# Kernel tuning notes

Hardware: AMD Instinct MI355X
Metric: run time of the kernel (lower is better)

The kernel has to match this reference:

```python
import jax, jax.numpy as jnp
import numpy as np

NDIR = 6      # build_tree.num_directions()
IDIM = 256
ODIM = 512
B, L, NCH = 8, 4096, 8192


def setup_inputs() -> dict:
    key = jax.random.key(0)
    ks = jax.random.split(key, 9)
    last = jax.random.normal(ks[0], (B, NCH, IDIM), dtype=jnp.float32)
    child_l = jax.random.randint(ks[1], (L,), 0, NCH, dtype=jnp.int32)
    child_r = jax.random.randint(ks[2], (L,), 0, NCH, dtype=jnp.int32)
    vec = jax.random.randint(ks[3], (B, L), 0, NCH, dtype=jnp.int32)
    drev = jax.random.randint(ks[4], (NCH,), 0, 2, dtype=jnp.int32)
    dmap = jax.random.randint(ks[5], (NCH,), 0, NDIR, dtype=jnp.int32)
    # merge FC params: ndir independent Linear(2*idim -> odim) + PReLU(init=relu_weight)
    scale = 1.0 / np.sqrt(2 * IDIM)
    W_merge = jax.random.uniform(ks[6], (NDIR, ODIM, 2 * IDIM), jnp.float32, -scale, scale)
    b_merge = jax.random.uniform(ks[7], (NDIR, ODIM), jnp.float32, -scale, scale)
    alpha_merge = jnp.full((NDIR,), 0.005, dtype=jnp.float32)  # PReLU weight (relu_weight)
    return {"last": last, "W_merge": W_merge, "b_merge": b_merge,
            "alpha_merge": alpha_merge, "child_l": child_l, "child_r": child_r,
            "vec": vec, "drev": drev, "dmap": dmap}


def reference(last, W_merge, b_merge, alpha_merge, child_l, child_r, vec, drev, dmap):
    # child gathers: [B, L, idim]
    lch = last[:, child_l]
    rch = last[:, child_r]
    # per-element direction-reverse blending
    d = drev[vec][:, :, None].astype(last.dtype)          # [B, L, 1]
    a = lch * (1.0 - d) + rch * d
    b = rch * (1.0 - d) + lch * d
    ans = jnp.concatenate([a, b], axis=-1)                # [B, L, 2*idim]
    # routed merge: compute all ndir linears, then select per element (ndir is small)
    y_all = jnp.einsum('bli,doi->bldo', ans, W_merge) + b_merge   # [B, L, ndir, odim]
    dir_idx = dmap[vec]                                   # [B, L] in [0, ndir)
    y = jnp.take_along_axis(y_all, dir_idx[:, :, None, None], axis=2)[:, :, 0]  # [B, L, odim]
    alpha = alpha_merge[dir_idx][:, :, None]              # per-element PReLU slope
    return jnp.where(y > 0, y, alpha * y)
```

## Files before the change

### kernel.cpp

```cpp
#include <hip/hip_runtime.h>
#include <hip/hip_bf16.h>

#define BB 8
#define LL 4096
#define NCH 8192
#define IDIM 256
#define KDIM 512
#define ODIM 512
#define NDIR 6
#define TOT (BB * LL)

typedef short short8 __attribute__((ext_vector_type(8)));
typedef float floatx4 __attribute__((ext_vector_type(4)));

#define WS_LAST_OFF (64 + 2 * TOT)
#define LAST_ELEMS (BB * NCH * IDIM)
#define W_ELEMS (NDIR * ODIM * KDIM)
#define N_LAST8 (LAST_ELEMS / 8)
#define N_W8 (W_ELEMS / 8)

__device__ inline void async_copy16(const void* g, void* l) {
  __builtin_amdgcn_global_load_lds(
      (const __attribute__((address_space(1))) void*)g,
      (__attribute__((address_space(3))) void*)l, 16, 0, 0);
}

__device__ inline void cvt8(const float* __restrict__ src,
                            __hip_bfloat16* __restrict__ dst, int i) {
  const floatx4* s = (const floatx4*)src;
  floatx4 a = s[2 * i];
  floatx4 b = s[2 * i + 1];
  union { short8 v; __hip_bfloat16 h[8]; } u;
  u.h[0] = __float2bfloat16(a[0]); u.h[1] = __float2bfloat16(a[1]);
  u.h[2] = __float2bfloat16(a[2]); u.h[3] = __float2bfloat16(a[3]);
  u.h[4] = __float2bfloat16(b[0]); u.h[5] = __float2bfloat16(b[1]);
  u.h[6] = __float2bfloat16(b[2]); u.h[7] = __float2bfloat16(b[3]);
  ((short8*)dst)[i] = u.v;
}

__global__ __launch_bounds__(256) void prep_kernel(
    const float* __restrict__ last, const float* __restrict__ W,
    const int* __restrict__ vec, const int* __restrict__ dmap,
    int* __restrict__ ws) {
  __hip_bfloat16* last_bf = (__hip_bfloat16*)(ws + WS_LAST_OFF);
  __hip_bfloat16* W_bf = last_bf + LAST_ELEMS;
  int gid = blockIdx.x * 256 + threadIdx.x;
  if (gid < N_LAST8) {
    cvt8(last, last_bf, gid);
  } else if (gid < N_LAST8 + N_W8) {
    cvt8(W, W_bf, gid - N_LAST8);
  } else {
    __shared__ int lcnt[8];
    int tid = threadIdx.x;
    if (tid < 8) lcnt[tid] = 0;
    __syncthreads();
    int lin = gid - (N_LAST8 + N_W8);
    int dir = dmap[vec[lin]] & 7;
    atomicAdd(&lcnt[dir], 1);
    __syncthreads();
    if (tid < 8 && lcnt[tid]) atomicAdd(&ws[tid], lcnt[tid]);
  }
}

__global__ void scan_kernel(int* __restrict__ ws) {
  if (threadIdx.x == 0) {
    int s = 0;
    for (int d = 0; d < 8; ++d) { ws[16 + d] = s; s += ws[d]; }
  }
}

__global__ __launch_bounds__(256) void scatter_kernel(
    const int* __restrict__ vec, const int* __restrict__ child_l,
    const int* __restrict__ child_r, const int* __restrict__ drev,
    const int* __restrict__ dmap, int* __restrict__ ws) {
  __shared__ int lcnt[8];
  __shared__ int gbase[8];
  int* fill = ws + 8;
  const int* base = ws + 16;
  int* idx = ws + 64;
  int* rows = ws + 64 + TOT;

  int tid = threadIdx.x;
  if (tid < 8) lcnt[tid] = 0;
  __syncthreads();

  int lin = blockIdx.x * 256 + tid;
  int l = lin & (LL - 1);
  int v = vec[lin];
  int dir = dmap[v] & 7;
  int sw = drev[v];
  int cl = child_l[l];
  int cr = child_r[l];
  int r0 = sw ? cr : cl;
  int r1 = sw ? cl : cr;
  int pos = atomicAdd(&lcnt[dir], 1);
  __syncthreads();
  if (tid < 8) gbase[tid] = lcnt[tid] ? atomicAdd(&fill[tid], lcnt[tid]) : 0;
  __syncthreads();
  int slot = base[dir] + gbase[dir] + pos;
  idx[slot] = lin;
  rows[slot] = r0 | (r1 << 16);
}

__global__ __launch_bounds__(256) void gemm_kernel(
    const float* __restrict__ bias, const float* __restrict__ alpha_m,
    const int* __restrict__ ws, float* __restrict__ out) {
  __shared__ __hip_bfloat16 Als[128 * 64];
  __shared__ __hip_bfloat16 Bls[128 * 64];

  const int mt = blockIdx.y;
  const int nt = blockIdx.x;
  int d = -1, count = 0, off = 0, m_base = 0;
  {
    int tb = 0;
    for (int dd = 0; dd < NDIR; ++dd) {
      int c = ws[dd];
      int ntile = (c + 127) >> 7;
      if (mt < tb + ntile) { d = dd; count = c; off = ws[16 + dd]; m_base = (mt - tb) * 128; break; }
      tb += ntile;
    }
  }
  if (d < 0) return;

  const int* idx = ws + 64;
  const int* rows = ws + 64 + TOT;
  const __hip_bfloat16* last_bf = (const __hip_bfloat16*)(ws + WS_LAST_OFF);
  const __hip_bfloat16* W_bf = last_bf + LAST_ELEMS;

  const int tid = threadIdx.x;
  const int wave = __builtin_amdgcn_readfirstlane(tid >> 6);
  const int lane = tid & 63;
  const int lane15 = lane & 15;
  const int quad = lane >> 4;
  const int wm = wave >> 1;
  const int wn = wave & 1;
  const int n_blk = nt * 128;

  const __hip_bfloat16* ap0[4];
  const __hip_bfloat16* ap1[4];
  const __hip_bfloat16* bp[4];
  int ldsrow[4];
#pragma unroll
  for (int i = 0; i < 4; ++i) {
    int sr = wave * 32 + i * 8 + (lane >> 3);
    ldsrow[i] = (wave * 32 + i * 8) * 64;
    int lr = m_base + sr;
    if (lr >= count) lr = count - 1;
    int lin = idx[off + lr] & (TOT - 1);
    int rr = rows[off + lr];
    int b = lin >> 12;
    int r0 = rr & (NCH - 1);
    int r1 = (rr >> 16) & (NCH - 1);
    int xu = ((lane & 7) ^ (sr & 7)) * 8;
    ap0[i] = last_bf + (long long)(b * NCH + r0) * IDIM + xu;
    ap1[i] = last_bf + (long long)(b * NCH + r1) * IDIM + xu;
    int xuB = xu;
    bp[i] = W_bf + (long long)(d * ODIM + n_blk + sr) * KDIM + xuB;
  }

  floatx4 acc[4][4] = {};
  const int lx = lane15 & 7;

#pragma unroll
  for (int kt = 0; kt < 8; ++kt) {
    __syncthreads();
    const int ko = (kt & 3) * 64;
#pragma unroll
    for (int i = 0; i < 4; ++i) {
      const __hip_bfloat16* ga = (kt < 4 ? ap0[i] : ap1[i]) + ko;
      async_copy16(ga, &Als[ldsrow[i]]);
    }
#pragma unroll
    for (int i = 0; i < 4; ++i) {
      async_copy16(bp[i] + kt * 64, &Bls[ldsrow[i]]);
    }
    __syncthreads();

#pragma unroll
    for (int s = 0; s < 2; ++s) {
      const int xcol = ((quad + 4 * s) ^ lx) * 8;
      short8 a[4], b[4];
#pragma unroll
      for (int i = 0; i < 4; ++i)
        a[i] = *(const short8*)&Als[(wm * 64 + i * 16 + lane15) * 64 + xcol];
#pragma unroll
      for (int j = 0; j < 4; ++j)
        b[j] = *(const short8*)&Bls[(wn * 64 + j * 16 + lane15) * 64 + xcol];
#pragma unroll
      for (int i = 0; i < 4; ++i)
#pragma unroll
        for (int j = 0; j < 4; ++j)
          acc[i][j] = __builtin_amdgcn_mfma_f32_16x16x32_bf16(a[i], b[j], acc[i][j], 0, 0, 0);
    }
  }

  const float alpha = alpha_m[d];
  float bj[4];
#pragma unroll
  for (int j = 0; j < 4; ++j)
    bj[j] = bias[d * ODIM + n_blk + wn * 64 + j * 16 + lane15];

#pragma unroll
  for (int i = 0; i < 4; ++i) {
#pragma unroll
    for (int reg = 0; reg < 4; ++reg) {
      int row_id = m_base + wm * 64 + i * 16 + quad * 4 + reg;
      if (row_id >= count) continue;
      int lin = idx[off + row_id] & (TOT - 1);
      float* orow = out + (long long)lin * ODIM + n_blk + wn * 64;
#pragma unroll
      for (int j = 0; j < 4; ++j) {
        float y = acc[i][j][reg] + bj[j];
        y = y > 0.f ? y : alpha * y;
        orow[j * 16 + lane15] = y;
      }
    }
  }
}

extern "C" void kernel_launch(void* const* d_in, const int* in_sizes, int n_in,
                              void* d_out, int out_size, void* d_ws, size_t ws_size,
                              hipStream_t stream) {
  const float* last = (const float*)d_in[0];
  const float* W = (const float*)d_in[1];
  const float* bias = (const float*)d_in[2];
  const float* alpha = (const float*)d_in[3];
  const int* child_l = (const int*)d_in[4];
  const int* child_r = (const int*)d_in[5];
  const int* vec = (const int*)d_in[6];
  const int* drev = (const int*)d_in[7];
  const int* dmap = (const int*)d_in[8];

  int* ws = (int*)d_ws;

  hipMemsetAsync(ws, 0, 64 * sizeof(int), stream);
  int prep_blocks = (N_LAST8 + N_W8 + TOT) / 256;
  prep_kernel<<<prep_blocks, 256, 0, stream>>>(last, W, vec, dmap, ws);
  scan_kernel<<<1, 64, 0, stream>>>(ws);
  scatter_kernel<<<TOT / 256, 256, 0, stream>>>(vec, child_l, child_r, drev, dmap, ws);
  dim3 grid(ODIM / 128, TOT / 128 + NDIR, 1);
  gemm_kernel<<<grid, 256, 0, stream>>>(bias, alpha, ws, (float*)d_out);
}
```

Baseline: 169.3 us.

## Pack gathered child rows into per-direction bf16 buffer and double-buffer GEMM K loop

Replaces full conversion of the input tensor to bf16 with a pack kernel that gathers only the needed left/right child rows, converts them, and writes them contiguously per direction slot. The scan and prep launches are removed, with slot positions computed directly in the scatter kernel using per-direction regions of size TOT. The GEMM now streams contiguous packed A rows with a two-stage LDS double buffer over 32-wide K tiles. This trades a large sparse workspace and an extra write of the gathered activations for simpler, coalesced GEMM loads and overlap of loads with MFMA work.

Measured after the change: 176.6 us. 1.04x slower.

```diff
diff --git a/kernel.cpp b/kernel.cpp
--- a/kernel.cpp
+++ b/kernel.cpp
@@ -13,60 +13,16 @@
 typedef short short8 __attribute__((ext_vector_type(8)));
 typedef float floatx4 __attribute__((ext_vector_type(4)));
 
-#define WS_LAST_OFF (64 + 2 * TOT)
-#define LAST_ELEMS (BB * NCH * IDIM)
+#define IDX_OFF (64 + 2 * TOT)
+#define PACKA_OFF_INTS (64 + (2 + NDIR) * TOT)
+#define PACKA_ELEMS ((long long)NDIR * TOT * KDIM)
 #define W_ELEMS (NDIR * ODIM * KDIM)
-#define N_LAST8 (LAST_ELEMS / 8)
 #define N_W8 (W_ELEMS / 8)
 
 __device__ inline void async_copy16(const void* g, void* l) {
   __builtin_amdgcn_global_load_lds(
       (const __attribute__((address_space(1))) void*)g,
       (__attribute__((address_space(3))) void*)l, 16, 0, 0);
-}
-
-__device__ inline void cvt8(const float* __restrict__ src,
-                            __hip_bfloat16* __restrict__ dst, int i) {
-  const floatx4* s = (const floatx4*)src;
-  floatx4 a = s[2 * i];
-  floatx4 b = s[2 * i + 1];
-  union { short8 v; __hip_bfloat16 h[8]; } u;
-  u.h[0] = __float2bfloat16(a[0]); u.h[1] = __float2bfloat16(a[1]);
-  u.h[2] = __float2bfloat16(a[2]); u.h[3] = __float2bfloat16(a[3]);
-  u.h[4] = __float2bfloat16(b[0]); u.h[5] = __float2bfloat16(b[1]);
-  u.h[6] = __float2bfloat16(b[2]); u.h[7] = __float2bfloat16(b[3]);
-  ((short8*)dst)[i] = u.v;
-}
-
-__global__ __launch_bounds__(256) void prep_kernel(
-    const float* __restrict__ last, const float* __restrict__ W,
-    const int* __restrict__ vec, const int* __restrict__ dmap,
-    int* __restrict__ ws) {
-  __hip_bfloat16* last_bf = (__hip_bfloat16*)(ws + WS_LAST_OFF);
-  __hip_bfloat16* W_bf = last_bf + LAST_ELEMS;
-  int gid = blockIdx.x * 256 + threadIdx.x;
-  if (gid < N_LAST8) {
-    cvt8(last, last_bf, gid);
-  } else if (gid < N_LAST8 + N_W8) {
-    cvt8(W, W_bf, gid - N_LAST8);
-  } else {
-    __shared__ int lcnt[8];
-    int tid = threadIdx.x;
-    if (tid < 8) lcnt[tid] = 0;
-    __syncthreads();
-    int lin = gid - (N_LAST8 + N_W8);
-    int dir = dmap[vec[lin]] & 7;
-    atomicAdd(&lcnt[dir], 1);
-    __syncthreads();
-    if (tid < 8 && lcnt[tid]) atomicAdd(&ws[tid], lcnt[tid]);
-  }
-}
-
-__global__ void scan_kernel(int* __restrict__ ws) {
-  if (threadIdx.x == 0) {
-    int s = 0;
-    for (int d = 0; d < 8; ++d) { ws[16 + d] = s; s += ws[d]; }
-  }
 }
 
 __global__ __launch_bounds__(256) void scatter_kernel(
@@ -75,11 +31,6 @@
     const int* __restrict__ dmap, int* __restrict__ ws) {
   __shared__ int lcnt[8];
   __shared__ int gbase[8];
-  int* fill = ws + 8;
-  const int* base = ws + 16;
-  int* idx = ws + 64;
-  int* rows = ws + 64 + TOT;
-
   int tid = threadIdx.x;
   if (tid < 8) lcnt[tid] = 0;
   __syncthreads();
@@ -95,37 +46,74 @@
   int r1 = sw ? cl : cr;
   int pos = atomicAdd(&lcnt[dir], 1);
   __syncthreads();
-  if (tid < 8) gbase[tid] = lcnt[tid] ? atomicAdd(&fill[tid], lcnt[tid]) : 0;
+  if (tid < 8) gbase[tid] = lcnt[tid] ? atomicAdd(&ws[tid], lcnt[tid]) : 0;
   __syncthreads();
-  int slot = base[dir] + gbase[dir] + pos;
-  idx[slot] = lin;
-  rows[slot] = r0 | (r1 << 16);
+  int slot = dir * TOT + gbase[dir] + pos;
+  ws[64 + lin] = slot;
+  ws[64 + TOT + lin] = r0 | (r1 << 16);
+}
+
+__global__ __launch_bounds__(256) void pack_kernel(
+    const float* __restrict__ last, const float* __restrict__ W,
+    int* __restrict__ ws) {
+  __hip_bfloat16* packedA = (__hip_bfloat16*)(ws + PACKA_OFF_INTS);
+  __hip_bfloat16* W_bf = packedA + PACKA_ELEMS;
+  int bid = blockIdx.x;
+  if (bid < TOT / 4) {
+    int tid = threadIdx.x;
+    int t = bid * 4 + (tid >> 6);
+    int L = tid & 63;
+    int slot = ws[64 + t];
+    int rr = ws[64 + TOT + t];
+    int b = t >> 12;
+    int r = (L < 32) ? (rr & (NCH - 1)) : ((rr >> 16) & (NCH - 1));
+    const floatx4* src =
+        (const floatx4*)(last + (long long)(b * NCH + r) * IDIM) + (L & 31) * 2;
+    floatx4 x0 = src[0];
+    floatx4 x1 = src[1];
+    union { short8 v; __hip_bfloat16 h[8]; } u;
+    u.h[0] = __float2bfloat16(x0[0]); u.h[1] = __float2bfloat16(x0[1]);
+    u.h[2] = __float2bfloat16(x0[2]); u.h[3] = __float2bfloat16(x0[3]);
+    u.h[4] = __float2bfloat16(x1[0]); u.h[5] = __float2bfloat16(x1[1]);
+    u.h[6] = __float2bfloat16(x1[2]); u.h[7] = __float2bfloat16(x1[3]);
+    ((short8*)(packedA + (long long)slot * KDIM + (L >> 5) * IDIM))[L & 31] = u.v;
+    if (L == 0) ws[IDX_OFF + slot] = t;
+  } else {
+    int gid = (bid - TOT / 4) * 256 + threadIdx.x;
+    const floatx4* s = (const floatx4*)W;
+    floatx4 a = s[2 * gid];
+    floatx4 b = s[2 * gid + 1];
+    union { short8 v; __hip_bfloat16 h[8]; } u;
+    u.h[0] = __float2bfloat16(a[0]); u.h[1] = __float2bfloat16(a[1]);
+    u.h[2] = __float2bfloat16(a[2]); u.h[3] = __float2bfloat16(a[3]);
+    u.h[4] = __float2bfloat16(b[0]); u.h[5] = __float2bfloat16(b[1]);
+    u.h[6] = __float2bfloat16(b[2]); u.h[7] = __float2bfloat16(b[3]);
+    ((short8*)W_bf)[gid] = u.v;
+  }
 }
 
 __global__ __launch_bounds__(256) void gemm_kernel(
     const float* __restrict__ bias, const float* __restrict__ alpha_m,
     const int* __restrict__ ws, float* __restrict__ out) {
-  __shared__ __hip_bfloat16 Als[128 * 64];
-  __shared__ __hip_bfloat16 Bls[128 * 64];
+  __shared__ __hip_bfloat16 Als[2][128 * 32];
+  __shared__ __hip_bfloat16 Bls[2][128 * 32];
 
   const int mt = blockIdx.y;
   const int nt = blockIdx.x;
-  int d = -1, count = 0, off = 0, m_base = 0;
+  int d = -1, count = 0, m_base = 0;
   {
     int tb = 0;
     for (int dd = 0; dd < NDIR; ++dd) {
       int c = ws[dd];
       int ntile = (c + 127) >> 7;
-      if (mt < tb + ntile) { d = dd; count = c; off = ws[16 + dd]; m_base = (mt - tb) * 128; break; }
+      if (mt < tb + ntile) { d = dd; count = c; m_base = (mt - tb) * 128; break; }
       tb += ntile;
     }
   }
   if (d < 0) return;
 
-  const int* idx = ws + 64;
-  const int* rows = ws + 64 + TOT;
-  const __hip_bfloat16* last_bf = (const __hip_bfloat16*)(ws + WS_LAST_OFF);
-  const __hip_bfloat16* W_bf = last_bf + LAST_ELEMS;
+  const __hip_bfloat16* packedA = (const __hip_bfloat16*)(ws + PACKA_OFF_INTS);
+  const __hip_bfloat16* W_bf = packedA + PACKA_ELEMS;
 
   const int tid = threadIdx.x;
   const int wave = __builtin_amdgcn_readfirstlane(tid >> 6);
@@ -136,62 +124,58 @@
   const int wn = wave & 1;
   const int n_blk = nt * 128;
 
-  const __hip_bfloat16* ap0[4];
-  const __hip_bfloat16* ap1[4];
-  const __hip_bfloat16* bp[4];
-  int ldsrow[4];
-#pragma unroll
-  for (int i = 0; i < 4; ++i) {
-    int sr = wave * 32 + i * 8 + (lane >> 3);
-    ldsrow[i] = (wave * 32 + i * 8) * 64;
-    int lr = m_base + sr;
-    if (lr >= count) lr = count - 1;
-    int lin = idx[off + lr] & (TOT - 1);
-    int rr = rows[off + lr];
-    int b = lin >> 12;
-    int r0 = rr & (NCH - 1);
-    int r1 = (rr >> 16) & (NCH - 1);
-    int xu = ((lane & 7) ^ (sr & 7)) * 8;
-    ap0[i] = last_bf + (long long)(b * NCH + r0) * IDIM + xu;
-    ap1[i] = last_bf + (long long)(b * NCH + r1) * IDIM + xu;
-    int xuB = xu;
-    bp[i] = W_bf + (long long)(d * ODIM + n_blk + sr) * KDIM + xuB;
+  const __hip_bfloat16* pa[2];
+  const __hip_bfloat16* pb[2];
+  int ldsbase[2];
+  {
+    int f = (lane >> 3) & 3;
+    int su = ((lane & 3) ^ f) * 8;
+#pragma unroll
+    for (int i = 0; i < 2; ++i) {
+      int sr = wave * 32 + i * 16 + (lane >> 2);
+      ldsbase[i] = (wave * 32 + i * 16) * 32;
+      int lr = m_base + sr;
+      if (lr >= count) lr = count - 1;
+      pa[i] = packedA + (long long)(d * TOT + lr) * KDIM + su;
+      pb[i] = W_bf + (long long)(d * ODIM + n_blk + sr) * KDIM + su;
+    }
   }
 
   floatx4 acc[4][4] = {};
-  const int lx = lane15 & 7;
-
-#pragma unroll
-  for (int kt = 0; kt < 8; ++kt) {
+  const int xq = (lane15 >> 1) & 3;
+  const int xcol = (quad ^ xq) * 8;
+
+#pragma unroll
+  for (int i = 0; i < 2; ++i) {
+    async_copy16(pa[i], &Als[0][ldsbase[i]]);
+    async_copy16(pb[i], &Bls[0][ldsbase[i]]);
+  }
+
+#pragma unroll
+  for (int kt = 0; kt < 16; ++kt) {
     __syncthreads();
-    const int ko = (kt & 3) * 64;
-#pragma unroll
-    for (int i = 0; i < 4; ++i) {
-      const __hip_bfloat16* ga = (kt < 4 ? ap0[i] : ap1[i]) + ko;
-      async_copy16(ga, &Als[ldsrow[i]]);
-    }
-#pragma unroll
-    for (int i = 0; i < 4; ++i) {
-      async_copy16(bp[i] + kt * 64, &Bls[ldsrow[i]]);
-    }
-    __syncthreads();
-
-#pragma unroll
-    for (int s = 0; s < 2; ++s) {
-      const int xcol = ((quad + 4 * s) ^ lx) * 8;
-      short8 a[4], b[4];
-#pragma unroll
-      for (int i = 0; i < 4; ++i)
-        a[i] = *(const short8*)&Als[(wm * 64 + i * 16 + lane15) * 64 + xcol];
+    if (kt < 15) {
+      const int nb = (kt + 1) & 1;
+      const int ko = (kt + 1) * 32;
+#pragma unroll
+      for (int i = 0; i < 2; ++i) {
+        async_copy16(pa[i] + ko, &Als[nb][ldsbase[i]]);
+        async_copy16(pb[i] + ko, &Bls[nb][ldsbase[i]]);
+      }
+    }
+    const int c = kt & 1;
+    short8 a[4], b[4];
+#pragma unroll
+    for (int i = 0; i < 4; ++i)
+      a[i] = *(const short8*)&Als[c][(wm * 64 + i * 16 + lane15) * 32 + xcol];
+#pragma unroll
+    for (int j = 0; j < 4; ++j)
+      b[j] = *(const short8*)&Bls[c][(wn * 64 + j * 16 + lane15) * 32 + xcol];
+#pragma unroll
+    for (int i = 0; i < 4; ++i)
 #pragma unroll
       for (int j = 0; j < 4; ++j)
-        b[j] = *(const short8*)&Bls[(wn * 64 + j * 16 + lane15) * 64 + xcol];
-#pragma unroll
-      for (int i = 0; i < 4; ++i)
-#pragma unroll
-        for (int j = 0; j < 4; ++j)
-          acc[i][j] = __builtin_amdgcn_mfma_f32_16x16x32_bf16(a[i], b[j], acc[i][j], 0, 0, 0);
-    }
+        acc[i][j] = __builtin_amdgcn_mfma_f32_16x16x32_bf16(a[i], b[j], acc[i][j], 0, 0, 0);
   }
 
   const float alpha = alpha_m[d];
@@ -206,8 +190,8 @@
     for (int reg = 0; reg < 4; ++reg) {
       int row_id = m_base + wm * 64 + i * 16 + quad * 4 + reg;
       if (row_id >= count) continue;
-      int lin = idx[off + row_id] & (TOT - 1);
-      float* orow = out + (long long)lin * ODIM + n_blk + wn * 64;
+      int t = ws[IDX_OFF + d * TOT + row_id] & (TOT - 1);
+      float* orow = out + (long long)t * ODIM + n_blk + wn * 64;
 #pragma unroll
       for (int j = 0; j < 4; ++j) {
         float y = acc[i][j][reg] + bj[j];
@@ -234,10 +218,8 @@
   int* ws = (int*)d_ws;
 
   hipMemsetAsync(ws, 0, 64 * sizeof(int), stream);
-  int prep_blocks = (N_LAST8 + N_W8 + TOT) / 256;
-  prep_kernel<<<prep_blocks, 256, 0, stream>>>(last, W, vec, dmap, ws);
-  scan_kernel<<<1, 64, 0, stream>>>(ws);
   scatter_kernel<<<TOT / 256, 256, 0, stream>>>(vec, child_l, child_r, drev, dmap, ws);
+  pack_kernel<<<TOT / 4 + N_W8 / 256, 256, 0, stream>>>(last, W, ws);
   dim3 grid(ODIM / 128, TOT / 128 + NDIR, 1);
   gemm_kernel<<<grid, 256, 0, stream>>>(bias, alpha, ws, (float*)d_out);
 }
```
